# Performance work log

Measured on AMD Instinct MI355X. Metric: run time of the kernel, lower is better.

The kernel has to match this reference:

```python
import jax, jax.numpy as jnp
import numpy as np

N, D, K = 65536, 128, 2048  # n_cells, latent_dim, nmb_prototypes


def setup_inputs() -> dict:
    key = jax.random.key(0)
    k1, k2, k3, k4, k5 = jax.random.split(key, 5)
    x = jax.random.normal(k1, (N, D), dtype=jnp.float32)
    # nn.Linear default init scale ~ 1/sqrt(fan_in)
    W_proto = jax.random.normal(k2, (K, D), dtype=jnp.float32) * (1.0 / np.sqrt(D))
    recon_loss = jax.random.uniform(k3, (), dtype=jnp.float32)
    kl_loss = jax.random.uniform(k4, (), dtype=jnp.float32)
    mmd_loss = jax.random.uniform(k5, (), dtype=jnp.float32)
    return {"x": x, "W_proto": W_proto, "recon_loss": recon_loss,
            "kl_loss": kl_loss, "mmd_loss": mmd_loss}


def _pairwise_dist(z, w):
    # torch.cdist(z, w, p=2) via the matmul expansion (use_mm_for_euclid_dist)
    zz = jnp.sum(z * z, axis=1, keepdims=True)       # [N, 1]
    ww = jnp.sum(w * w, axis=1, keepdims=True).T     # [1, K]
    sq = zz + ww - 2.0 * (z @ w.T)                   # [N, K]
    return jnp.sqrt(jnp.maximum(sq, 0.0))


def reference(x, W_proto, recon_loss, kl_loss, mmd_loss):
    # cvae loss combination (compute_cvae_loss, calc_alpha_coeff = 0.5)
    cvae_loss = recon_loss + 0.5 * kl_loss + mmd_loss
    # F.normalize(x, dim=1, p=2): x / max(||x||_2, eps)
    nrm = jnp.maximum(jnp.linalg.norm(x, axis=1, keepdims=True), 1e-12)
    z = x / nrm                                      # [N, D]
    # self.prototypes(x): Linear without bias
    logits = z @ W_proto.T                           # [N, K]
    # prototype_decoding_loss: one NxK distance matrix reduced two ways
    dist = _pairwise_dist(z, W_proto)                # [N, K]
    propagation = jnp.mean(jnp.min(dist, axis=1))    # nearest prototype per cell
    emb_similarity = jnp.mean(jnp.min(dist, axis=0))  # nearest cell per prototype
    # forward returns (x, x, prototypes(x), cvae_loss, (prop, emb_sim)); x duplicated
    return (z, logits, cvae_loss, propagation, emb_similarity)
```

## Files before the change

kernel.cpp:

```cpp
#include <hip/hip_runtime.h>
#include <hip/hip_bf16.h>
#include <math.h>

#define N_CELLS 65536
#define D_DIM   128
#define K_PROTO 2048

typedef __attribute__((ext_vector_type(8))) short bf16x8;
typedef __attribute__((ext_vector_type(4))) float f32x4;

__device__ __forceinline__ unsigned int f2bf(float f) {
  unsigned int u = __float_as_uint(f);
  return ((u + 0x7FFFu + ((u >> 16) & 1u)) >> 16) & 0xFFFFu;
}

__global__ __launch_bounds__(256) void normalize_k(
    const float* __restrict__ x, float* __restrict__ z,
    unsigned int* __restrict__ zb) {
  int tid = threadIdx.x;
  int sub = tid & 31;
  int row = blockIdx.x * 8 + (tid >> 5);
  const f32x4* xr = (const f32x4*)(x + (size_t)row * D_DIM);
  f32x4 v = xr[sub];
  float s = v.x * v.x + v.y * v.y + v.z * v.z + v.w * v.w;
  #pragma unroll
  for (int off = 1; off < 32; off <<= 1) s += __shfl_xor(s, off, 64);
  float inv = 1.0f / fmaxf(sqrtf(s), 1e-12f);
  f32x4 zv = v * inv;
  __builtin_nontemporal_store(zv, (f32x4*)(z + (size_t)row * D_DIM) + sub);
  unsigned int lo = (f2bf(zv.y) << 16) | f2bf(zv.x);
  unsigned int h2 = (f2bf(zv.w) << 16) | f2bf(zv.z);
  unsigned long long pk = ((unsigned long long)h2 << 32) | lo;
  *((unsigned long long*)(zb + (size_t)row * (D_DIM / 2)) + sub) = pk;
}

__global__ __launch_bounds__(256) void wprep_k(
    const float* __restrict__ W, unsigned int* __restrict__ wb,
    float* __restrict__ ww,
    const float* __restrict__ recon, const float* __restrict__ kl,
    const float* __restrict__ mmd, float* __restrict__ scal) {
  if (blockIdx.x == 0 && threadIdx.x == 0) {
    scal[0] = recon[0] + 0.5f * kl[0] + mmd[0];
  }
  int tid = threadIdx.x;
  int sub = tid & 31;
  int row = blockIdx.x * 8 + (tid >> 5);
  const f32x4* wr = (const f32x4*)(W + (size_t)row * D_DIM);
  f32x4 v = wr[sub];
  float s = v.x * v.x + v.y * v.y + v.z * v.z + v.w * v.w;
  #pragma unroll
  for (int off = 1; off < 32; off <<= 1) s += __shfl_xor(s, off, 64);
  if (sub == 0) ww[row] = s;
  unsigned int lo = (f2bf(v.y) << 16) | f2bf(v.x);
  unsigned int h2 = (f2bf(v.w) << 16) | f2bf(v.z);
  unsigned long long pk = ((unsigned long long)h2 << 32) | lo;
  *((unsigned long long*)(wb + (size_t)row * (D_DIM / 2)) + sub) = pk;
}

__global__ __launch_bounds__(256) void gemm_k(
    const unsigned short* __restrict__ zb, const unsigned short* __restrict__ wb,
    const float* __restrict__ ww, float* __restrict__ logits,
    float* __restrict__ rowmin_part, float* __restrict__ colmax_part) {
  __shared__ float cs[128 * 128];
  __shared__ float rmin[2][128];
  __shared__ float cmx[2][128];

  int bid = blockIdx.x;
  int mt  = (bid & 7) * 64 + (bid >> 5);
  int ntg = (bid >> 3) & 3;

  int tid  = threadIdx.x;
  int lane = tid & 63;
  int wid  = tid >> 6;
  int wrow = (wid >> 1) * 64;
  int wcol = (wid & 1) * 64;
  int l15  = lane & 15;
  int hi   = lane >> 4;

  const char* Abase = (const char*)zb + ((size_t)(mt * 128 + wrow + l15) * 256 + hi * 16);
  bf16x8 afr[4][4];
  #pragma unroll
  for (int i = 0; i < 4; ++i)
    #pragma unroll
    for (int kk = 0; kk < 4; ++kk)
      afr[i][kk] = *(const bf16x8*)(Abase + i * 4096 + kk * 64);

  float vrm[4];
  #pragma unroll
  for (int i = 0; i < 4; ++i) vrm[i] = 1e30f;

  #pragma unroll
  for (int t = 0; t < 4; ++t) {
    int nt = ntg * 4 + t;
    const char* Bbase = (const char*)wb + ((size_t)(nt * 128 + wcol + l15) * 256 + hi * 16);

    f32x4 acc[4][4];
    #pragma unroll
    for (int i = 0; i < 4; ++i)
      #pragma unroll
      for (int j = 0; j < 4; ++j)
        acc[i][j] = f32x4{0.f, 0.f, 0.f, 0.f};

    #pragma unroll
    for (int kk = 0; kk < 4; ++kk) {
      bf16x8 b[4];
      #pragma unroll
      for (int j = 0; j < 4; ++j) b[j] = *(const bf16x8*)(Bbase + j * 4096 + kk * 64);
      #pragma unroll
      for (int i = 0; i < 4; ++i)
        #pragma unroll
        for (int j = 0; j < 4; ++j)
          acc[i][j] = __builtin_amdgcn_mfma_f32_16x16x32_bf16(b[j], afr[i][kk], acc[i][j], 0, 0, 0);
    }

    int gcolbase = nt * 128 + wcol;
    f32x4 wwj[4];
    #pragma unroll
    for (int j = 0; j < 4; ++j)
      wwj[j] = *(const f32x4*)(ww + gcolbase + j * 16 + hi * 4);

    #pragma unroll
    for (int i = 0; i < 4; ++i) {
      float vmin = 1e30f;
      #pragma unroll
      for (int j = 0; j < 4; ++j)
        #pragma unroll
        for (int r = 0; r < 4; ++r) vmin = fminf(vmin, wwj[j][r] - 2.0f * acc[i][j][r]);
      vmin = fminf(vmin, __shfl_xor(vmin, 16, 64));
      vmin = fminf(vmin, __shfl_xor(vmin, 32, 64));
      vrm[i] = fminf(vrm[i], vmin);
    }

    __syncthreads();

    #pragma unroll
    for (int j = 0; j < 4; ++j) {
      f32x4 m = acc[0][j];
      #pragma unroll
      for (int i = 1; i < 4; ++i)
        #pragma unroll
        for (int r = 0; r < 4; ++r) m[r] = fmaxf(m[r], acc[i][j][r]);
      #pragma unroll
      for (int s2 = 1; s2 < 16; s2 <<= 1)
        #pragma unroll
        for (int r = 0; r < 4; ++r) m[r] = fmaxf(m[r], __shfl_xor(m[r], s2, 64));
      if (l15 == 0)
        *(f32x4*)&cmx[wid >> 1][wcol + j * 16 + hi * 4] = m;
    }

    #pragma unroll
    for (int i = 0; i < 4; ++i) {
      int row = wrow + i * 16 + l15;
      #pragma unroll
      for (int j = 0; j < 4; ++j) {
        int g  = (wcol >> 2) + j * 4 + hi;
        int pg = g ^ ((row & 7) << 2);
        *(f32x4*)((char*)cs + row * 512 + pg * 16) = acc[i][j];
      }
    }
    __syncthreads();

    if (tid >= 128) {
      int c = tid - 128;
      colmax_part[(size_t)mt * K_PROTO + nt * 128 + c] =
          fmaxf(cmx[0][c], cmx[1][c]);
    }

    {
      int l31  = lane & 31;
      int rsub = lane >> 5;
      #pragma unroll
      for (int it = 0; it < 16; ++it) {
        int row = it * 8 + wid * 2 + rsub;
        int pg  = l31 ^ ((row & 7) << 2);
        f32x4 c = *(const f32x4*)((const char*)cs + row * 512 + pg * 16);
        size_t grow = (size_t)mt * 128 + row;
        __builtin_nontemporal_store(c, (f32x4*)(logits + grow * K_PROTO + nt * 128 + l31 * 4));
      }
    }
  }

  if (hi == 0) {
    #pragma unroll
    for (int i = 0; i < 4; ++i) rmin[wid & 1][wrow + i * 16 + l15] = vrm[i];
  }
  __syncthreads();
  if (tid < 128) {
    rowmin_part[(size_t)ntg * N_CELLS + mt * 128 + tid] =
        fminf(rmin[0][tid], rmin[1][tid]);
  }
}

__global__ __launch_bounds__(1024) void prop1_k(
    const float* __restrict__ rowmin_part, float* __restrict__ prop_part) {
  __shared__ float sbuf[16];
  int slot = blockIdx.x * 1024 + threadIdx.x;
  f32x4 v = *(const f32x4*)(rowmin_part + (size_t)slot * 4);
  #pragma unroll
  for (int p = 1; p < 4; ++p) {
    f32x4 u = *(const f32x4*)(rowmin_part + (size_t)p * N_CELLS + (size_t)slot * 4);
    #pragma unroll
    for (int r = 0; r < 4; ++r) v[r] = fminf(v[r], u[r]);
  }
  float s = 0.f;
  #pragma unroll
  for (int r = 0; r < 4; ++r) s += sqrtf(fmaxf(1.0f + v[r], 0.0f));
  #pragma unroll
  for (int off = 1; off < 64; off <<= 1) s += __shfl_xor(s, off, 64);
  int wv = threadIdx.x >> 6, lane = threadIdx.x & 63;
  if (lane == 0) sbuf[wv] = s;
  __syncthreads();
  if (threadIdx.x == 0) {
    float t = 0.f;
    #pragma unroll
    for (int w = 0; w < 16; ++w) t += sbuf[w];
    prop_part[blockIdx.x] = t;
  }
}

__global__ __launch_bounds__(1024) void emb1_k(
    const float* __restrict__ colmax_part, const float* __restrict__ ww,
    float* __restrict__ emb_part) {
  __shared__ float buf[8][128];
  __shared__ float sbuf[2];
  int t   = threadIdx.x;
  int col = blockIdx.x * 128 + (t & 127);
  int seg = t >> 7;
  float m = -1e30f;
  for (int k = 0; k < 64; ++k)
    m = fmaxf(m, colmax_part[(size_t)(seg * 64 + k) * K_PROTO + col]);
  buf[seg][t & 127] = m;
  __syncthreads();
  if (t < 128) {
    float tot = buf[0][t];
    #pragma unroll
    for (int s2 = 1; s2 < 8; ++s2) tot = fmaxf(tot, buf[s2][t]);
    float val = sqrtf(fmaxf(1.0f + ww[col] - 2.0f * tot, 0.0f));
    #pragma unroll
    for (int off = 1; off < 64; off <<= 1) val += __shfl_xor(val, off, 64);
    if ((t & 63) == 0) sbuf[t >> 6] = val;
  }
  __syncthreads();
  if (t == 0) emb_part[blockIdx.x] = sbuf[0] + sbuf[1];
}

__global__ __launch_bounds__(64) void final_k(
    const float* __restrict__ prop_part, const float* __restrict__ emb_part,
    float* __restrict__ scal) {
  if (threadIdx.x == 0) {
    float p = 0.f, e = 0.f;
    #pragma unroll
    for (int i = 0; i < 16; ++i) { p += prop_part[i]; e += emb_part[i]; }
    scal[1] = p * (1.0f / N_CELLS);
    scal[2] = e * (1.0f / K_PROTO);
  }
}

extern "C" void kernel_launch(void* const* d_in, const int* in_sizes, int n_in,
                              void* d_out, int out_size, void* d_ws, size_t ws_size,
                              hipStream_t stream) {
  const float* x     = (const float*)d_in[0];
  const float* W     = (const float*)d_in[1];
  const float* recon = (const float*)d_in[2];
  const float* kl    = (const float*)d_in[3];
  const float* mmd   = (const float*)d_in[4];

  float* out    = (float*)d_out;
  float* z      = out;
  float* logits = out + (size_t)N_CELLS * D_DIM;
  float* scal   = logits + (size_t)N_CELLS * K_PROTO;

  char* ws = (char*)d_ws;
  unsigned int* zb = (unsigned int*)ws;
  size_t off = (size_t)N_CELLS * D_DIM * 2;
  unsigned int* wb = (unsigned int*)(ws + off);
  off += (size_t)K_PROTO * D_DIM * 2;
  float* ww = (float*)(ws + off);
  off += (size_t)K_PROTO * 4;
  float* rowmin_part = (float*)(ws + off);
  off += (size_t)4 * N_CELLS * 4;
  float* colmax_part = (float*)(ws + off);
  off += (size_t)512 * K_PROTO * 4;
  float* prop_part = (float*)(ws + off);
  off += 16 * 4;
  float* emb_part = (float*)(ws + off);

  normalize_k<<<N_CELLS / 8, 256, 0, stream>>>(x, z, zb);
  wprep_k<<<K_PROTO / 8, 256, 0, stream>>>(W, wb, ww, recon, kl, mmd, scal);
  gemm_k<<<2048, 256, 0, stream>>>(
      (const unsigned short*)zb, (const unsigned short*)wb, ww, logits,
      rowmin_part, colmax_part);
  prop1_k<<<16, 1024, 0, stream>>>(rowmin_part, prop_part);
  emb1_k<<<16, 1024, 0, stream>>>(colmax_part, ww, emb_part);
  final_k<<<1, 64, 0, stream>>>(prop_part, emb_part, scal);
}
```

Measured before the change: 219.8 us.

## Give each GEMM block a full row tile over all prototypes, use LDS-only barriers

The GEMM grid changes from 2048 blocks, each covering a quarter of the prototype columns, to 512 blocks that each loop over all 16 column tiles. Row minima are therefore finished inside the kernel, which removes the 4-way partial rowmin buffer and its reduction in prop1_k. __syncthreads is replaced with a custom barrier that waits only on LDS counters, so the outstanding nontemporal global stores are not drained at each barrier. The costs are fewer blocks (512 on a 256-CU GPU, so less latency hiding and a tail effect), a loop that is no longer unrolled, and the loss of the previous block-index swizzle for L2 locality.

```diff
diff --git a/kernel.cpp b/kernel.cpp
--- a/kernel.cpp
+++ b/kernel.cpp
@@ -12,6 +12,14 @@
 __device__ __forceinline__ unsigned int f2bf(float f) {
   unsigned int u = __float_as_uint(f);
   return ((u + 0x7FFFu + ((u >> 16) & 1u)) >> 16) & 0xFFFFu;
+}
+
+__device__ __forceinline__ void lds_barrier() {
+  __builtin_amdgcn_sched_barrier(0);
+  asm volatile("s_waitcnt lgkmcnt(0)" ::: "memory");
+  __builtin_amdgcn_sched_barrier(0);
+  __builtin_amdgcn_s_barrier();
+  __builtin_amdgcn_sched_barrier(0);
 }
 
 __global__ __launch_bounds__(256) void normalize_k(
@@ -60,14 +68,12 @@
 __global__ __launch_bounds__(256) void gemm_k(
     const unsigned short* __restrict__ zb, const unsigned short* __restrict__ wb,
     const float* __restrict__ ww, float* __restrict__ logits,
-    float* __restrict__ rowmin_part, float* __restrict__ colmax_part) {
+    float* __restrict__ rowmin_final, float* __restrict__ colmax_part) {
   __shared__ float cs[128 * 128];
   __shared__ float rmin[2][128];
   __shared__ float cmx[2][128];
 
-  int bid = blockIdx.x;
-  int mt  = (bid & 7) * 64 + (bid >> 5);
-  int ntg = (bid >> 3) & 3;
+  int mt = blockIdx.x;
 
   int tid  = threadIdx.x;
   int lane = tid & 63;
@@ -76,6 +82,8 @@
   int wcol = (wid & 1) * 64;
   int l15  = lane & 15;
   int hi   = lane >> 4;
+  int l31  = lane & 31;
+  int rsub = lane >> 5;
 
   const char* Abase = (const char*)zb + ((size_t)(mt * 128 + wrow + l15) * 256 + hi * 16);
   bf16x8 afr[4][4];
@@ -89,9 +97,7 @@
   #pragma unroll
   for (int i = 0; i < 4; ++i) vrm[i] = 1e30f;
 
-  #pragma unroll
-  for (int t = 0; t < 4; ++t) {
-    int nt = ntg * 4 + t;
+  for (int nt = 0; nt < 16; ++nt) {
     const char* Bbase = (const char*)wb + ((size_t)(nt * 128 + wcol + l15) * 256 + hi * 16);
 
     f32x4 acc[4][4];
@@ -131,7 +137,7 @@
       vrm[i] = fminf(vrm[i], vmin);
     }
 
-    __syncthreads();
+    lds_barrier();
 
     #pragma unroll
     for (int j = 0; j < 4; ++j) {
@@ -158,7 +164,8 @@
         *(f32x4*)((char*)cs + row * 512 + pg * 16) = acc[i][j];
       }
     }
-    __syncthreads();
+
+    lds_barrier();
 
     if (tid >= 128) {
       int c = tid - 128;
@@ -166,17 +173,13 @@
           fmaxf(cmx[0][c], cmx[1][c]);
     }
 
-    {
-      int l31  = lane & 31;
-      int rsub = lane >> 5;
-      #pragma unroll
-      for (int it = 0; it < 16; ++it) {
-        int row = it * 8 + wid * 2 + rsub;
-        int pg  = l31 ^ ((row & 7) << 2);
-        f32x4 c = *(const f32x4*)((const char*)cs + row * 512 + pg * 16);
-        size_t grow = (size_t)mt * 128 + row;
-        __builtin_nontemporal_store(c, (f32x4*)(logits + grow * K_PROTO + nt * 128 + l31 * 4));
-      }
+    #pragma unroll
+    for (int it = 0; it < 16; ++it) {
+      int row = it * 8 + wid * 2 + rsub;
+      int pg  = l31 ^ ((row & 7) << 2);
+      f32x4 c = *(const f32x4*)((const char*)cs + row * 512 + pg * 16);
+      size_t grow = (size_t)mt * 128 + row;
+      __builtin_nontemporal_store(c, (f32x4*)(logits + grow * K_PROTO + nt * 128 + l31 * 4));
     }
   }
 
@@ -184,24 +187,17 @@
     #pragma unroll
     for (int i = 0; i < 4; ++i) rmin[wid & 1][wrow + i * 16 + l15] = vrm[i];
   }
-  __syncthreads();
+  lds_barrier();
   if (tid < 128) {
-    rowmin_part[(size_t)ntg * N_CELLS + mt * 128 + tid] =
-        fminf(rmin[0][tid], rmin[1][tid]);
+    rowmin_final[mt * 128 + tid] = fminf(rmin[0][tid], rmin[1][tid]);
   }
 }
 
 __global__ __launch_bounds__(1024) void prop1_k(
-    const float* __restrict__ rowmin_part, float* __restrict__ prop_part) {
+    const float* __restrict__ rowmin_final, float* __restrict__ prop_part) {
   __shared__ float sbuf[16];
   int slot = blockIdx.x * 1024 + threadIdx.x;
-  f32x4 v = *(const f32x4*)(rowmin_part + (size_t)slot * 4);
-  #pragma unroll
-  for (int p = 1; p < 4; ++p) {
-    f32x4 u = *(const f32x4*)(rowmin_part + (size_t)p * N_CELLS + (size_t)slot * 4);
-    #pragma unroll
-    for (int r = 0; r < 4; ++r) v[r] = fminf(v[r], u[r]);
-  }
+  f32x4 v = *(const f32x4*)(rowmin_final + (size_t)slot * 4);
   float s = 0.f;
   #pragma unroll
   for (int r = 0; r < 4; ++r) s += sqrtf(fmaxf(1.0f + v[r], 0.0f));
@@ -277,8 +273,8 @@
   off += (size_t)K_PROTO * D_DIM * 2;
   float* ww = (float*)(ws + off);
   off += (size_t)K_PROTO * 4;
-  float* rowmin_part = (float*)(ws + off);
-  off += (size_t)4 * N_CELLS * 4;
+  float* rowmin_final = (float*)(ws + off);
+  off += (size_t)N_CELLS * 4;
   float* colmax_part = (float*)(ws + off);
   off += (size_t)512 * K_PROTO * 4;
   float* prop_part = (float*)(ws + off);
@@ -287,10 +283,10 @@
 
   normalize_k<<<N_CELLS / 8, 256, 0, stream>>>(x, z, zb);
   wprep_k<<<K_PROTO / 8, 256, 0, stream>>>(W, wb, ww, recon, kl, mmd, scal);
-  gemm_k<<<2048, 256, 0, stream>>>(
+  gemm_k<<<N_CELLS / 128, 256, 0, stream>>>(
       (const unsigned short*)zb, (const unsigned short*)wb, ww, logits,
-      rowmin_part, colmax_part);
-  prop1_k<<<16, 1024, 0, stream>>>(rowmin_part, prop_part);
+      rowmin_final, colmax_part);
+  prop1_k<<<16, 1024, 0, stream>>>(rowmin_final, prop_part);
   emb1_k<<<16, 1024, 0, stream>>>(colmax_part, ww, emb_part);
   final_k<<<1, 64, 0, stream>>>(prop_part, emb_part, scal);
 }
```

After: 232.5 us. 1.06x slower.

## Prefetch next B tile into registers and use LDS-only barriers in gemm

Applied to the files above, without the earlier changes.

The GEMM now loads the next prototype tile's B fragments and ww norms into registers while the current tile's epilogue runs, so global loads overlap the LDS reductions and logits stores. __syncthreads is replaced by a barrier that waits only on LDS counters (lgkmcnt), so outstanding global loads and stores no longer stall it. Launch bounds are raised to ask for two waves per SIMD. The extra 16 prefetch registers increase register pressure, which could cause spills or lower occupancy under the new bound.

```diff
diff --git a/kernel.cpp b/kernel.cpp
--- a/kernel.cpp
+++ b/kernel.cpp
@@ -12,6 +12,14 @@
 __device__ __forceinline__ unsigned int f2bf(float f) {
   unsigned int u = __float_as_uint(f);
   return ((u + 0x7FFFu + ((u >> 16) & 1u)) >> 16) & 0xFFFFu;
+}
+
+__device__ __forceinline__ void lds_barrier() {
+  __builtin_amdgcn_sched_barrier(0);
+  asm volatile("s_waitcnt lgkmcnt(0)" ::: "memory");
+  __builtin_amdgcn_sched_barrier(0);
+  __builtin_amdgcn_s_barrier();
+  __builtin_amdgcn_sched_barrier(0);
 }
 
 __global__ __launch_bounds__(256) void normalize_k(
@@ -57,7 +65,7 @@
   *((unsigned long long*)(wb + (size_t)row * (D_DIM / 2)) + sub) = pk;
 }
 
-__global__ __launch_bounds__(256) void gemm_k(
+__global__ __launch_bounds__(256, 2) void gemm_k(
     const unsigned short* __restrict__ zb, const unsigned short* __restrict__ wb,
     const float* __restrict__ ww, float* __restrict__ logits,
     float* __restrict__ rowmin_part, float* __restrict__ colmax_part) {
@@ -76,6 +84,8 @@
   int wcol = (wid & 1) * 64;
   int l15  = lane & 15;
   int hi   = lane >> 4;
+  int l31  = lane & 31;
+  int rsub = lane >> 5;
 
   const char* Abase = (const char*)zb + ((size_t)(mt * 128 + wrow + l15) * 256 + hi * 16);
   bf16x8 afr[4][4];
@@ -89,10 +99,24 @@
   #pragma unroll
   for (int i = 0; i < 4; ++i) vrm[i] = 1e30f;
 
+  bf16x8 bfr[16];
+  f32x4  wwj[4];
+  {
+    int nt0 = ntg * 4;
+    const char* Bbase = (const char*)wb + ((size_t)(nt0 * 128 + wcol + l15) * 256 + hi * 16);
+    #pragma unroll
+    for (int j = 0; j < 4; ++j)
+      #pragma unroll
+      for (int kk = 0; kk < 4; ++kk)
+        bfr[j * 4 + kk] = *(const bf16x8*)(Bbase + j * 4096 + kk * 64);
+    #pragma unroll
+    for (int j = 0; j < 4; ++j)
+      wwj[j] = *(const f32x4*)(ww + nt0 * 128 + wcol + j * 16 + hi * 4);
+  }
+
   #pragma unroll
   for (int t = 0; t < 4; ++t) {
     int nt = ntg * 4 + t;
-    const char* Bbase = (const char*)wb + ((size_t)(nt * 128 + wcol + l15) * 256 + hi * 16);
 
     f32x4 acc[4][4];
     #pragma unroll
@@ -102,22 +126,12 @@
         acc[i][j] = f32x4{0.f, 0.f, 0.f, 0.f};
 
     #pragma unroll
-    for (int kk = 0; kk < 4; ++kk) {
-      bf16x8 b[4];
-      #pragma unroll
-      for (int j = 0; j < 4; ++j) b[j] = *(const bf16x8*)(Bbase + j * 4096 + kk * 64);
+    for (int kk = 0; kk < 4; ++kk)
       #pragma unroll
       for (int i = 0; i < 4; ++i)
         #pragma unroll
         for (int j = 0; j < 4; ++j)
-          acc[i][j] = __builtin_amdgcn_mfma_f32_16x16x32_bf16(b[j], afr[i][kk], acc[i][j], 0, 0, 0);
-    }
-
-    int gcolbase = nt * 128 + wcol;
-    f32x4 wwj[4];
-    #pragma unroll
-    for (int j = 0; j < 4; ++j)
-      wwj[j] = *(const f32x4*)(ww + gcolbase + j * 16 + hi * 4);
+          acc[i][j] = __builtin_amdgcn_mfma_f32_16x16x32_bf16(bfr[j * 4 + kk], afr[i][kk], acc[i][j], 0, 0, 0);
 
     #pragma unroll
     for (int i = 0; i < 4; ++i) {
@@ -131,7 +145,21 @@
       vrm[i] = fminf(vrm[i], vmin);
     }
 
-    __syncthreads();
+    if (t < 3) {
+      int ntn = nt + 1;
+      const char* Bbase = (const char*)wb + ((size_t)(ntn * 128 + wcol + l15) * 256 + hi * 16);
+      #pragma unroll
+      for (int j = 0; j < 4; ++j)
+        #pragma unroll
+        for (int kk = 0; kk < 4; ++kk)
+          bfr[j * 4 + kk] = *(const bf16x8*)(Bbase + j * 4096 + kk * 64);
+      #pragma unroll
+      for (int j = 0; j < 4; ++j)
+        wwj[j] = *(const f32x4*)(ww + ntn * 128 + wcol + j * 16 + hi * 4);
+      __builtin_amdgcn_sched_barrier(0);
+    }
+
+    lds_barrier();
 
     #pragma unroll
     for (int j = 0; j < 4; ++j) {
@@ -158,7 +186,8 @@
         *(f32x4*)((char*)cs + row * 512 + pg * 16) = acc[i][j];
       }
     }
-    __syncthreads();
+
+    lds_barrier();
 
     if (tid >= 128) {
       int c = tid - 128;
@@ -166,17 +195,13 @@
           fmaxf(cmx[0][c], cmx[1][c]);
     }
 
-    {
-      int l31  = lane & 31;
-      int rsub = lane >> 5;
-      #pragma unroll
-      for (int it = 0; it < 16; ++it) {
-        int row = it * 8 + wid * 2 + rsub;
-        int pg  = l31 ^ ((row & 7) << 2);
-        f32x4 c = *(const f32x4*)((const char*)cs + row * 512 + pg * 16);
-        size_t grow = (size_t)mt * 128 + row;
-        __builtin_nontemporal_store(c, (f32x4*)(logits + grow * K_PROTO + nt * 128 + l31 * 4));
-      }
+    #pragma unroll
+    for (int it = 0; it < 16; ++it) {
+      int row = it * 8 + wid * 2 + rsub;
+      int pg  = l31 ^ ((row & 7) << 2);
+      f32x4 c = *(const f32x4*)((const char*)cs + row * 512 + pg * 16);
+      size_t grow = (size_t)mt * 128 + row;
+      __builtin_nontemporal_store(c, (f32x4*)(logits + grow * K_PROTO + nt * 128 + l31 * 4));
     }
   }
 
@@ -184,7 +209,7 @@
     #pragma unroll
     for (int i = 0; i < 4; ++i) rmin[wid & 1][wrow + i * 16 + l15] = vrm[i];
   }
-  __syncthreads();
+  lds_barrier();
   if (tid < 128) {
     rowmin_part[(size_t)ntg * N_CELLS + mt * 128 + tid] =
         fminf(rmin[0][tid], rmin[1][tid]);
```

After: 229.3 us. 1.04x slower.
